# Optimization experiments

Measured on AMD Instinct MI355X. Metric: run time of the kernel, lower is better.

## Reference

```python
import jax, jax.numpy as jnp
import numpy as np

COMMITMENT_COST = 0.25


def setup_inputs() -> dict:
    key = jax.random.key(0)
    k1, k2 = jax.random.split(key)
    B, H, W, D, K = 64, 32, 32, 64, 512
    inputs = jax.random.normal(k1, (B, H, W, D), dtype=jnp.float32)
    # VarianceScaling(): truncated normal with stddev ~ sqrt(1/fan_in); plain normal scaled is fine as init
    embeddings = jax.random.normal(k2, (D, K), dtype=jnp.float32) * np.float32(1.0 / np.sqrt(D))
    return {"inputs": inputs, "embeddings": embeddings}


def reference(inputs, embeddings):
    D = embeddings.shape[0]
    flat = inputs.reshape(-1, D)  # [N, D]
    distances = (
        jnp.sum(flat * flat, axis=1, keepdims=True)
        - 2.0 * (flat @ embeddings)
        + jnp.sum(embeddings * embeddings, axis=0, keepdims=True)
    )
    encoding_indices = jnp.argmin(distances, axis=1)  # [N]
    # one-hot @ embeddings.T is just a gather of rows of embeddings.T
    quantized = jnp.take(embeddings.T, encoding_indices, axis=0).reshape(inputs.shape)
    loss = (
        jnp.mean(jnp.square(jax.lax.stop_gradient(quantized) - inputs))
        + COMMITMENT_COST * jnp.mean(jnp.square(quantized - jax.lax.stop_gradient(inputs)))
    )
    # straight-through estimator
    quantized_st = inputs + jax.lax.stop_gradient(quantized - inputs)
    indices = encoding_indices.reshape(inputs.shape[:-1])
    return quantized_st, indices, loss
```

## Files before the change

### kernel.cpp

```cpp
#include <hip/hip_runtime.h>
#include <stdint.h>


#define DDIM 64
#define KCODES 512

typedef __bf16 bf16x8 __attribute__((ext_vector_type(8)));
typedef float f32x4 __attribute__((ext_vector_type(4)));


__device__ __forceinline__ void split3(float f, __bf16& h1, __bf16& h2,
                                       __bf16& h3) {
  h1 = (__bf16)f;
  float r1 = f - (float)h1;
  h2 = (__bf16)r1;
  float r2 = r1 - (float)h2;
  h3 = (__bf16)r2;
}

__global__ void vq_prep_m(const float* __restrict__ x_in,
                          const float* __restrict__ w,
                          bf16x8* __restrict__ xa1, bf16x8* __restrict__ xa2,
                          bf16x8* __restrict__ xa3, bf16x8* __restrict__ wb,
                          float* __restrict__ wT, float* __restrict__ wsq,
                          float* __restrict__ xsq,
                          float* __restrict__ loss_out) {
  __shared__ float xs[64][65];
  const int b = blockIdx.x, t = threadIdx.x;
  if (b < 1024) {
    const float4* src = (const float4*)(x_in + (size_t)b * 4096);
#pragma unroll
    for (int i = 0; i < 4; ++i) {
      float4 v = src[i * 256 + t];
      int e = (i * 256 + t) * 4;
      int pt = e >> 6, d = e & 63;
      xs[pt][d] = v.x; xs[pt][d + 1] = v.y;
      xs[pt][d + 2] = v.z; xs[pt][d + 3] = v.w;
    }
    __syncthreads();
    const int grp = t >> 6, L = t & 63, quad = L >> 4, col = L & 15;
    const int ptl = grp * 16 + col;
    const int nblk = b * 4 + grp;
    float ssq = 0.f;
#pragma unroll
    for (int h = 0; h < 2; ++h) {
      bf16x8 v1, v2, v3;
#pragma unroll
      for (int j = 0; j < 8; ++j) {
        float f = xs[ptl][quad * 8 + 32 * h + j];
        ssq = fmaf(f, f, ssq);
        __bf16 h1, h2, h3; split3(f, h1, h2, h3);
        v1[j] = h1; v2[j] = h2; v3[j] = h3;
      }
      int idx = (nblk * 2 + h) * 64 + L;
      xa1[idx] = v1; xa2[idx] = v2; xa3[idx] = v3;
    }
    ssq += __shfl_xor(ssq, 16, 64);
    ssq += __shfl_xor(ssq, 32, 64);
    if (quad == 0) xsq[b * 64 + ptl] = ssq;
  } else if (b < 1056) {
    const int ctg = b - 1024;
    const int u = t >> 6, L = t & 63, quad = L >> 4, col = L & 15;
    if (u < 2) {
      const int h = u;
      bf16x8 v1, v2, v3;
#pragma unroll
      for (int j = 0; j < 8; ++j) {
        float f = w[(quad * 8 + 32 * h + j) * KCODES + ctg * 16 + col];
        __bf16 h1, h2, h3; split3(f, h1, h2, h3);
        v1[j] = h1; v2[j] = h2; v3[j] = h3;
      }
      int idx = (ctg * 2 + h) * 64 + L;
      wb[idx] = v1; wb[4096 + idx] = v2; wb[8192 + idx] = v3;
    }
  } else {
    int g = (b - 1056) * 256 + t;
    int d = g >> 9, k = g & 511;
    wT[k * DDIM + d] = w[g];
    if (g < KCODES) {
      float s = 0.f;
      for (int dd = 0; dd < DDIM; ++dd) {
        float tv = w[dd * KCODES + g];
        s = fmaf(tv, tv, s);
      }
      wsq[g] = s;
    }
    if (g == 0) *loss_out = 0.f;
  }
}

__global__ __launch_bounds__(256, 2)
void vq_mfma(const bf16x8* __restrict__ xa1, const bf16x8* __restrict__ xa2,
             const bf16x8* __restrict__ xa3, const bf16x8* __restrict__ wb,
             const float* __restrict__ wsq, const float* __restrict__ xsq,
             float* __restrict__ out_idx, float* __restrict__ loss_out) {
  __shared__ bf16x8 ldsb[3072];
  __shared__ unsigned long long sm_key[128];
  __shared__ float sm_loss[128];

  const int t = threadIdx.x, b = blockIdx.x;
  const int wv = t >> 6, L = t & 63, quad = L >> 4, col = L & 15;
  const int nblk0 = b * 8 + wv * 2;

  bf16x8 a[2][3][2];
#pragma unroll
  for (int as = 0; as < 2; ++as) {
    int base = (nblk0 + as) * 2;
#pragma unroll
    for (int h = 0; h < 2; ++h) {
      a[as][0][h] = xa1[(base + h) * 64 + L];
      a[as][1][h] = xa2[(base + h) * 64 + L];
      a[as][2][h] = xa3[(base + h) * 64 + L];
    }
  }

  float best[2][4];
  int bidx[2][4];
#pragma unroll
  for (int as = 0; as < 2; ++as)
#pragma unroll
    for (int r = 0; r < 4; ++r) { best[as][r] = 3.0e38f; bidx[as][r] = 0; }

#pragma unroll 1
  for (int ph = 0; ph < 4; ++ph) {
    if (ph) __syncthreads();
#pragma unroll
    for (int i = 0; i < 12; ++i) {
      int idx = i * 256 + t;
      int chunk = idx >> 6, Ls = idx & 63;
      int ct = chunk / 6, r6 = chunk % 6;
      int h = r6 / 3, s = r6 % 3;
      ldsb[chunk * 64 + Ls] =
          wb[s * 4096 + ((ph * 8 + ct) * 2 + h) * 64 + Ls];
    }
    __syncthreads();
#pragma unroll 1
    for (int ct = 0; ct < 8; ++ct) {
      f32x4 acc0 = {0.f, 0.f, 0.f, 0.f};
      f32x4 acc1 = {0.f, 0.f, 0.f, 0.f};
#pragma unroll
      for (int h = 0; h < 2; ++h) {
        bf16x8 b0 = ldsb[(ct * 6 + h * 3 + 0) * 64 + L];
        bf16x8 b1 = ldsb[(ct * 6 + h * 3 + 1) * 64 + L];
        bf16x8 b2 = ldsb[(ct * 6 + h * 3 + 2) * 64 + L];
        acc0 = __builtin_amdgcn_mfma_f32_16x16x32_bf16(a[0][0][h], b0, acc0, 0, 0, 0);
        acc1 = __builtin_amdgcn_mfma_f32_16x16x32_bf16(a[1][0][h], b0, acc1, 0, 0, 0);
        acc0 = __builtin_amdgcn_mfma_f32_16x16x32_bf16(a[0][0][h], b1, acc0, 0, 0, 0);
        acc1 = __builtin_amdgcn_mfma_f32_16x16x32_bf16(a[1][0][h], b1, acc1, 0, 0, 0);
        acc0 = __builtin_amdgcn_mfma_f32_16x16x32_bf16(a[0][1][h], b0, acc0, 0, 0, 0);
        acc1 = __builtin_amdgcn_mfma_f32_16x16x32_bf16(a[1][1][h], b0, acc1, 0, 0, 0);
        acc0 = __builtin_amdgcn_mfma_f32_16x16x32_bf16(a[0][1][h], b1, acc0, 0, 0, 0);
        acc1 = __builtin_amdgcn_mfma_f32_16x16x32_bf16(a[1][1][h], b1, acc1, 0, 0, 0);
        acc0 = __builtin_amdgcn_mfma_f32_16x16x32_bf16(a[0][0][h], b2, acc0, 0, 0, 0);
        acc1 = __builtin_amdgcn_mfma_f32_16x16x32_bf16(a[1][0][h], b2, acc1, 0, 0, 0);
        acc0 = __builtin_amdgcn_mfma_f32_16x16x32_bf16(a[0][2][h], b0, acc0, 0, 0, 0);
        acc1 = __builtin_amdgcn_mfma_f32_16x16x32_bf16(a[1][2][h], b0, acc1, 0, 0, 0);
      }
      int code = ph * 128 + ct * 16 + col;
      float wq = wsq[code];
#pragma unroll
      for (int r = 0; r < 4; ++r) {
        float d0 = fmaf(acc0[r], -2.0f, wq);
        if (d0 < best[0][r]) { best[0][r] = d0; bidx[0][r] = code; }
        float d1 = fmaf(acc1[r], -2.0f, wq);
        if (d1 < best[1][r]) { best[1][r] = d1; bidx[1][r] = code; }
      }
    }
  }

#pragma unroll
  for (int as = 0; as < 2; ++as) {
#pragma unroll
    for (int r = 0; r < 4; ++r) {
      unsigned int ub = __float_as_uint(best[as][r]);
      ub = (ub & 0x80000000u) ? ~ub : (ub | 0x80000000u);
      unsigned long long key = ((unsigned long long)ub << 32) |
                               (unsigned long long)(unsigned int)bidx[as][r];
#pragma unroll
      for (int off = 1; off < 16; off <<= 1) {
        unsigned long long o = __shfl_xor(key, off, 64);
        key = o < key ? o : key;
      }
      if (col == 0)
        sm_key[wv * 32 + as * 16 + quad * 4 + r] = key;
    }
  }
  __syncthreads();

  if (t < 128) {
    unsigned long long k = sm_key[t];
    unsigned int idx = (unsigned int)k;
    out_idx[(size_t)b * 128 + t] = (float)idx;
    unsigned int u = (unsigned int)(k >> 32);
    u = (u & 0x80000000u) ? (u & 0x7FFFFFFFu) : ~u;
    sm_loss[t] =
        (__uint_as_float(u) + xsq[(size_t)b * 128 + t]) * (1.25f / 4194304.0f);
  }
  __syncthreads();
  if (t < 64) {
    float s = sm_loss[t] + sm_loss[t + 64];
#pragma unroll
    for (int off = 32; off > 0; off >>= 1) s += __shfl_down(s, off);
    if (t == 0) atomicAdd(loss_out, s);
  }
}

__global__ void vq_gather(const float* __restrict__ idx_f,
                          const float* __restrict__ wT,
                          float4* __restrict__ out_q) {
  int g4 = blockIdx.x * 256 + threadIdx.x;
  int n = g4 >> 4, d4 = g4 & 15;
  unsigned int idx = (unsigned int)idx_f[n];
  out_q[g4] = ((const float4*)(wT + (size_t)idx * DDIM))[d4];
}


__global__ void vq_prep(const float* __restrict__ w, float* __restrict__ wT,
                        float* __restrict__ wsq, float* __restrict__ loss_out) {
  int g = blockIdx.x * 256 + threadIdx.x;
  int d = g >> 9, k = g & 511;
  wT[k * DDIM + d] = w[g];
  if (g < KCODES) {
    float s = 0.f;
    for (int dd = 0; dd < DDIM; ++dd) {
      float t = w[dd * KCODES + g];
      s = fmaf(t, t, s);
    }
    wsq[g] = s;
  }
  if (g == 0) *loss_out = 0.f;
}

__global__ __launch_bounds__(512, 8)
void vq_main(const float* __restrict__ x_in, const float* __restrict__ w,
             const float* __restrict__ wT, const float* __restrict__ wsq,
             float* __restrict__ out_q, float* __restrict__ out_idx,
             float* __restrict__ loss_out) {
  __shared__ float xs[DDIM][65];
  __shared__ unsigned long long sm_key[8][64];
  __shared__ unsigned int sm_idx[64];
  __shared__ float sm_sx[64];
  __shared__ float sm_loss[64];

  const int t = threadIdx.x;
  const int pb = blockIdx.x;
  const int wv = __builtin_amdgcn_readfirstlane(t >> 6);
  const int lane = t & 63;

  {
    const float4* src = (const float4*)(x_in + (size_t)pb * 4096);
#pragma unroll
    for (int i = 0; i < 2; ++i) {
      int e4 = i * 512 + t;
      float4 v = src[e4];
      int e = e4 << 2;
      int pt = e >> 6, d = e & 63;
      xs[d][pt] = v.x; xs[d + 1][pt] = v.y;
      xs[d + 2][pt] = v.z; xs[d + 3][pt] = v.w;
    }
  }
  __syncthreads();

  const int kbase = wv << 6;
  float best = 3.0e38f;
  int bidx = 0;
  float sx = 0.f;

#pragma unroll 1
  for (int kb = 0; kb < 2; ++kb) {
    const int k0 = kbase + (kb << 5);
    const float* wp = w + k0;
    float acc[32];
#pragma unroll
    for (int c = 0; c < 32; ++c) acc[c] = 0.f;
#pragma unroll 1
    for (int d8 = 0; d8 < 8; ++d8) {
      float xv[8];
#pragma unroll
      for (int dd = 0; dd < 8; ++dd) xv[dd] = xs[(d8 << 3) + dd][lane];
      if (wv == 0 && kb == 0) {
#pragma unroll
        for (int dd = 0; dd < 8; ++dd) sx = fmaf(xv[dd], xv[dd], sx);
      }
#pragma unroll
      for (int dd = 0; dd < 8; ++dd) {
        const float* wd = wp + (((d8 << 3) + dd) << 9);
#pragma unroll
        for (int c = 0; c < 32; ++c) acc[c] = fmaf(wd[c], xv[dd], acc[c]);
      }
    }
#pragma unroll
    for (int c = 0; c < 32; ++c) {
      float dist = fmaf(acc[c], -2.0f, wsq[k0 + c]);
      if (dist < best) { best = dist; bidx = k0 + c; }
    }
  }

  unsigned int ub = __float_as_uint(best);
  ub = (ub & 0x80000000u) ? ~ub : (ub | 0x80000000u);
  sm_key[wv][lane] =
      ((unsigned long long)ub << 32) | (unsigned long long)(unsigned int)bidx;
  if (wv == 0) sm_sx[lane] = sx;
  __syncthreads();

  if (t < 64) {
    unsigned long long k = sm_key[0][t];
#pragma unroll
    for (int wi = 1; wi < 8; ++wi) {
      unsigned long long k2 = sm_key[wi][t];
      k = k2 < k ? k2 : k;
    }
    unsigned int idx = (unsigned int)k;
    sm_idx[t] = idx;
    out_idx[((size_t)pb << 6) + t] = (float)idx;
    unsigned int u = (unsigned int)(k >> 32);
    u = (u & 0x80000000u) ? (u & 0x7FFFFFFFu) : ~u;
    sm_loss[t] = (__uint_as_float(u) + sm_sx[t]) * (1.25f / 4194304.0f);
  }
  __syncthreads();

  float4* dst = (float4*)(out_q + (size_t)pb * 4096);
#pragma unroll
  for (int i = 0; i < 2; ++i) {
    int e4 = i * 512 + t;
    int p2 = e4 >> 4, d4 = e4 & 15;
    unsigned int idx = sm_idx[p2];
    dst[e4] = ((const float4*)(wT + (size_t)idx * DDIM))[d4];
  }

  if (t < 64) {
    float s = sm_loss[t];
#pragma unroll
    for (int off = 32; off > 0; off >>= 1) s += __shfl_down(s, off);
    if (t == 0) atomicAdd(loss_out, s);
  }
}

extern "C" void kernel_launch(void* const* d_in, const int* in_sizes, int n_in,
                              void* d_out, int out_size, void* d_ws, size_t ws_size,
                              hipStream_t stream) {
  const float* x = (const float*)d_in[0];
  const float* w = (const float*)d_in[1];

  float* out_q = (float*)d_out;
  float* out_idx = out_q + 4194304;
  float* loss_out = out_q + 4259840;

  char* ws = (char*)d_ws;
  if (ws_size >= 8980480) {
    bf16x8* xa1 = (bf16x8*)d_out;
    bf16x8* xa2 = (bf16x8*)((char*)d_out + 8388608);
    bf16x8* xa3 = (bf16x8*)(ws);
    bf16x8* wbp = (bf16x8*)(ws + 8388608);
    float* wT = (float*)(ws + 8585216);
    float* xsq = (float*)(ws + 8716288);
    float* wsq = (float*)(ws + 8978432);
    vq_prep_m<<<1184, 256, 0, stream>>>(x, w, xa1, xa2, xa3, wbp, wT, wsq,
                                        xsq, loss_out);
    vq_mfma<<<512, 256, 0, stream>>>(xa1, xa2, xa3, wbp, wsq, xsq, out_idx,
                                     loss_out);
    vq_gather<<<4096, 256, 0, stream>>>(out_idx, wT, (float4*)out_q);
  } else {
    float* wT = (float*)(ws);
    float* wsq = (float*)(ws + 131072);
    vq_prep<<<128, 256, 0, stream>>>(w, wT, wsq, loss_out);
    vq_main<<<1024, 512, 0, stream>>>(x, w, wT, wsq, out_q, out_idx,
                                      loss_out);
  }
}
```

Measured before the change: 113.2 us.

## Fuse input bf16 splitting and codebook gather into the MFMA kernel

Input rows are now read straight from x inside the MFMA kernel, which splits them into three bf16 parts and computes their squared norms in registers. The prep kernel no longer writes and the main kernel no longer rereads the split-input workspace (three bf16 copies of x plus xsq). The separate gather kernel is folded into the MFMA kernel's epilogue, which writes quantized rows using indices held in shared memory. This removes one launch and a large amount of global traffic. In exchange, the per-lane x loads in the main kernel are strided rather than coalesced through LDS.

```diff
diff --git a/kernel.cpp b/kernel.cpp
--- a/kernel.cpp
+++ b/kernel.cpp
@@ -18,63 +18,26 @@
   h3 = (__bf16)r2;
 }
 
-__global__ void vq_prep_m(const float* __restrict__ x_in,
-                          const float* __restrict__ w,
-                          bf16x8* __restrict__ xa1, bf16x8* __restrict__ xa2,
-                          bf16x8* __restrict__ xa3, bf16x8* __restrict__ wb,
+__global__ void vq_prep_m(const float* __restrict__ w,
+                          bf16x8* __restrict__ wb,
                           float* __restrict__ wT, float* __restrict__ wsq,
-                          float* __restrict__ xsq,
                           float* __restrict__ loss_out) {
-  __shared__ float xs[64][65];
   const int b = blockIdx.x, t = threadIdx.x;
-  if (b < 1024) {
-    const float4* src = (const float4*)(x_in + (size_t)b * 4096);
-#pragma unroll
-    for (int i = 0; i < 4; ++i) {
-      float4 v = src[i * 256 + t];
-      int e = (i * 256 + t) * 4;
-      int pt = e >> 6, d = e & 63;
-      xs[pt][d] = v.x; xs[pt][d + 1] = v.y;
-      xs[pt][d + 2] = v.z; xs[pt][d + 3] = v.w;
-    }
-    __syncthreads();
-    const int grp = t >> 6, L = t & 63, quad = L >> 4, col = L & 15;
-    const int ptl = grp * 16 + col;
-    const int nblk = b * 4 + grp;
-    float ssq = 0.f;
-#pragma unroll
-    for (int h = 0; h < 2; ++h) {
-      bf16x8 v1, v2, v3;
-#pragma unroll
-      for (int j = 0; j < 8; ++j) {
-        float f = xs[ptl][quad * 8 + 32 * h + j];
-        ssq = fmaf(f, f, ssq);
-        __bf16 h1, h2, h3; split3(f, h1, h2, h3);
-        v1[j] = h1; v2[j] = h2; v3[j] = h3;
-      }
-      int idx = (nblk * 2 + h) * 64 + L;
-      xa1[idx] = v1; xa2[idx] = v2; xa3[idx] = v3;
-    }
-    ssq += __shfl_xor(ssq, 16, 64);
-    ssq += __shfl_xor(ssq, 32, 64);
-    if (quad == 0) xsq[b * 64 + ptl] = ssq;
-  } else if (b < 1056) {
-    const int ctg = b - 1024;
-    const int u = t >> 6, L = t & 63, quad = L >> 4, col = L & 15;
-    if (u < 2) {
-      const int h = u;
-      bf16x8 v1, v2, v3;
-#pragma unroll
-      for (int j = 0; j < 8; ++j) {
-        float f = w[(quad * 8 + 32 * h + j) * KCODES + ctg * 16 + col];
-        __bf16 h1, h2, h3; split3(f, h1, h2, h3);
-        v1[j] = h1; v2[j] = h2; v3[j] = h3;
-      }
-      int idx = (ctg * 2 + h) * 64 + L;
-      wb[idx] = v1; wb[4096 + idx] = v2; wb[8192 + idx] = v3;
-    }
+  if (b < 16) {
+    const int c = b * 256 + t;
+    const int ctg = c >> 7;
+    const int h = (c >> 6) & 1;
+    const int L = c & 63, quad = L >> 4, col = L & 15;
+    bf16x8 v1, v2, v3;
+#pragma unroll
+    for (int j = 0; j < 8; ++j) {
+      float f = w[(quad * 8 + 32 * h + j) * KCODES + ctg * 16 + col];
+      __bf16 h1, h2, h3; split3(f, h1, h2, h3);
+      v1[j] = h1; v2[j] = h2; v3[j] = h3;
+    }
+    wb[c] = v1; wb[4096 + c] = v2; wb[8192 + c] = v3;
   } else {
-    int g = (b - 1056) * 256 + t;
+    int g = (b - 16) * 256 + t;
     int d = g >> 9, k = g & 511;
     wT[k * DDIM + d] = w[g];
     if (g < KCODES) {
@@ -90,28 +53,42 @@
 }
 
 __global__ __launch_bounds__(256, 2)
-void vq_mfma(const bf16x8* __restrict__ xa1, const bf16x8* __restrict__ xa2,
-             const bf16x8* __restrict__ xa3, const bf16x8* __restrict__ wb,
-             const float* __restrict__ wsq, const float* __restrict__ xsq,
-             float* __restrict__ out_idx, float* __restrict__ loss_out) {
+void vq_mfma(const float* __restrict__ x_in, const bf16x8* __restrict__ wb,
+             const float* __restrict__ wsq, const float* __restrict__ wT,
+             float* __restrict__ out_q, float* __restrict__ out_idx,
+             float* __restrict__ loss_out) {
   __shared__ bf16x8 ldsb[3072];
   __shared__ unsigned long long sm_key[128];
+  __shared__ float sm_xsq[128];
+  __shared__ unsigned int sm_idx[128];
   __shared__ float sm_loss[128];
 
   const int t = threadIdx.x, b = blockIdx.x;
   const int wv = t >> 6, L = t & 63, quad = L >> 4, col = L & 15;
-  const int nblk0 = b * 8 + wv * 2;
 
   bf16x8 a[2][3][2];
 #pragma unroll
   for (int as = 0; as < 2; ++as) {
-    int base = (nblk0 + as) * 2;
+    const float* xr =
+        x_in + ((size_t)b * 128 + (wv * 2 + as) * 16 + col) * DDIM + quad * 8;
+    float ssq = 0.f;
 #pragma unroll
     for (int h = 0; h < 2; ++h) {
-      a[as][0][h] = xa1[(base + h) * 64 + L];
-      a[as][1][h] = xa2[(base + h) * 64 + L];
-      a[as][2][h] = xa3[(base + h) * 64 + L];
-    }
+      float4 p0 = *(const float4*)(xr + 32 * h);
+      float4 p1 = *(const float4*)(xr + 32 * h + 4);
+      float f[8] = {p0.x, p0.y, p0.z, p0.w, p1.x, p1.y, p1.z, p1.w};
+      bf16x8 v1, v2, v3;
+#pragma unroll
+      for (int j = 0; j < 8; ++j) {
+        ssq = fmaf(f[j], f[j], ssq);
+        __bf16 h1, h2, h3; split3(f[j], h1, h2, h3);
+        v1[j] = h1; v2[j] = h2; v3[j] = h3;
+      }
+      a[as][0][h] = v1; a[as][1][h] = v2; a[as][2][h] = v3;
+    }
+    ssq += __shfl_xor(ssq, 16, 64);
+    ssq += __shfl_xor(ssq, 32, 64);
+    if (quad == 0) sm_xsq[wv * 32 + as * 16 + col] = ssq;
   }
 
   float best[2][4];
@@ -123,15 +100,14 @@
 
 #pragma unroll 1
   for (int ph = 0; ph < 4; ++ph) {
-    if (ph) __syncthreads();
+    __syncthreads();
 #pragma unroll
     for (int i = 0; i < 12; ++i) {
       int idx = i * 256 + t;
       int chunk = idx >> 6, Ls = idx & 63;
       int ct = chunk / 6, r6 = chunk % 6;
       int h = r6 / 3, s = r6 % 3;
-      ldsb[chunk * 64 + Ls] =
-          wb[s * 4096 + ((ph * 8 + ct) * 2 + h) * 64 + Ls];
+      ldsb[chunk * 64 + Ls] = wb[s * 4096 + ((ph * 8 + ct) * 2 + h) * 64 + Ls];
     }
     __syncthreads();
 #pragma unroll 1
@@ -190,28 +166,29 @@
   if (t < 128) {
     unsigned long long k = sm_key[t];
     unsigned int idx = (unsigned int)k;
+    sm_idx[t] = idx;
     out_idx[(size_t)b * 128 + t] = (float)idx;
     unsigned int u = (unsigned int)(k >> 32);
     u = (u & 0x80000000u) ? (u & 0x7FFFFFFFu) : ~u;
-    sm_loss[t] =
-        (__uint_as_float(u) + xsq[(size_t)b * 128 + t]) * (1.25f / 4194304.0f);
-  }
-  __syncthreads();
+    sm_loss[t] = (__uint_as_float(u) + sm_xsq[t]) * (1.25f / 4194304.0f);
+  }
+  __syncthreads();
+
+  float4* dst = (float4*)(out_q + (size_t)b * 8192);
+#pragma unroll
+  for (int i = 0; i < 8; ++i) {
+    int e4 = i * 256 + t;
+    int p2 = e4 >> 4, d4 = e4 & 15;
+    unsigned int idx = sm_idx[p2];
+    dst[e4] = ((const float4*)(wT + (size_t)idx * DDIM))[d4];
+  }
+
   if (t < 64) {
     float s = sm_loss[t] + sm_loss[t + 64];
 #pragma unroll
     for (int off = 32; off > 0; off >>= 1) s += __shfl_down(s, off);
     if (t == 0) atomicAdd(loss_out, s);
   }
-}
-
-__global__ void vq_gather(const float* __restrict__ idx_f,
-                          const float* __restrict__ wT,
-                          float4* __restrict__ out_q) {
-  int g4 = blockIdx.x * 256 + threadIdx.x;
-  int n = g4 >> 4, d4 = g4 & 15;
-  unsigned int idx = (unsigned int)idx_f[n];
-  out_q[g4] = ((const float4*)(wT + (size_t)idx * DDIM))[d4];
 }
 
 
@@ -347,19 +324,13 @@
   float* loss_out = out_q + 4259840;
 
   char* ws = (char*)d_ws;
-  if (ws_size >= 8980480) {
-    bf16x8* xa1 = (bf16x8*)d_out;
-    bf16x8* xa2 = (bf16x8*)((char*)d_out + 8388608);
-    bf16x8* xa3 = (bf16x8*)(ws);
-    bf16x8* wbp = (bf16x8*)(ws + 8388608);
-    float* wT = (float*)(ws + 8585216);
-    float* xsq = (float*)(ws + 8716288);
-    float* wsq = (float*)(ws + 8978432);
-    vq_prep_m<<<1184, 256, 0, stream>>>(x, w, xa1, xa2, xa3, wbp, wT, wsq,
-                                        xsq, loss_out);
-    vq_mfma<<<512, 256, 0, stream>>>(xa1, xa2, xa3, wbp, wsq, xsq, out_idx,
+  if (ws_size >= 329728) {
+    bf16x8* wbp = (bf16x8*)(ws);
+    float* wT = (float*)(ws + 196608);
+    float* wsq = (float*)(ws + 327680);
+    vq_prep_m<<<144, 256, 0, stream>>>(w, wbp, wT, wsq, loss_out);
+    vq_mfma<<<512, 256, 0, stream>>>(x, wbp, wsq, wT, out_q, out_idx,
                                      loss_out);
-    vq_gather<<<4096, 256, 0, stream>>>(out_idx, wT, (float4*)out_q);
   } else {
     float* wT = (float*)(ws);
     float* wsq = (float*)(ws + 131072);
```

After: 109.5 us. 1.03x faster.
